# Performance work log

Measured on AMD Instinct MI355X. Metric: run time of the kernel, lower is better.

## Reference

```python
import jax, jax.numpy as jnp
import numpy as np

HIDDEN = 1024
N_EXPERTS = 8
TOP_K = 2
INTER = 1408
NORM_TOPK = False


def setup_inputs() -> dict:
    key = jax.random.key(0)
    ks = jax.random.split(key, 5)
    B, S = 4, 2048
    scale_h = 1.0 / np.sqrt(HIDDEN)
    scale_i = 1.0 / np.sqrt(INTER)
    return {
        "hidden_states": jax.random.normal(ks[0], (B, S, HIDDEN), dtype=jnp.float32),
        "gate_w": jax.random.normal(ks[1], (N_EXPERTS, HIDDEN), dtype=jnp.float32) * scale_h,  # router
        "w_gate": jax.random.normal(ks[2], (N_EXPERTS, HIDDEN, INTER), dtype=jnp.float32) * scale_h,
        "w_up": jax.random.normal(ks[3], (N_EXPERTS, HIDDEN, INTER), dtype=jnp.float32) * scale_h,
        "w_down": jax.random.normal(ks[4], (N_EXPERTS, INTER, HIDDEN), dtype=jnp.float32) * scale_i,
    }


def reference(hidden_states, gate_w, w_gate, w_up, w_down):
    B, S, H = hidden_states.shape
    x = hidden_states.reshape(-1, H)                     # [T, H]
    T = x.shape[0]

    router_logits = x @ gate_w.T                          # [T, E]
    probs = jax.nn.softmax(router_logits.astype(jnp.float32), axis=-1)
    topk_w, topk_idx = jax.lax.top_k(probs, TOP_K)        # [T, K]
    if NORM_TOPK:
        topk_w = topk_w / jnp.sum(topk_w, axis=-1, keepdims=True)
    topk_w = topk_w.astype(x.dtype)

    # Scatter top-k weights into dense [T, E] combine weights (0 for unselected).
    weights = jnp.zeros((T, N_EXPERTS), dtype=x.dtype)
    weights = weights.at[jnp.arange(T)[:, None], topk_idx].set(topk_w)

    # Dense grouped SwiGLU over all experts; combine masks out unrouted pairs.
    g = jnp.einsum('th,ehi->eti', x, w_gate)              # [E, T, I]
    u = jnp.einsum('th,ehi->eti', x, w_up)                # [E, T, I]
    y = jnp.einsum('eti,eih->eth', jax.nn.silu(g) * u, w_down)  # [E, T, H]
    final = jnp.einsum('eth,te->th', y, weights)          # [T, H]

    return final.reshape(B, S, H), router_logits
```

## Files before the change

### kernel.cpp

```cpp
#include <hip/hip_runtime.h>
#include <hip/hip_bf16.h>
#include <math.h>

#define T_TOK 8192
#define HID   1024
#define NE    8
#define TOPKN 2
#define INTER 1408
#define NROWS (T_TOK*TOPKN)
#define MAXWL 144
#define RBLK  256

typedef __attribute__((ext_vector_type(8))) __bf16 bf16x8;
typedef __attribute__((ext_vector_type(4))) float f32x4;
typedef __attribute__((ext_vector_type(4))) unsigned int u32x4;

__device__ __forceinline__ unsigned short f2bf(float f) {
    unsigned int u = __builtin_bit_cast(unsigned int, f);
    unsigned int lsb = (u >> 16) & 1u;
    u += 0x7fffu + lsb;
    return (unsigned short)(u >> 16);
}

__device__ __forceinline__ void gl2lds16(const void* g, void* l) {
    __builtin_amdgcn_global_load_lds(
        (const __attribute__((address_space(1))) unsigned int*)g,
        (__attribute__((address_space(3))) unsigned int*)l, 16, 0, 0);
}

__global__ __launch_bounds__(256) void moe_router(
    const float* __restrict__ x, const float* __restrict__ gate_w,
    unsigned short* __restrict__ xb, float* __restrict__ logits_out,
    int* __restrict__ topk_idx, float* __restrict__ topk_w,
    int* __restrict__ hist_g)
{
    __shared__ int lh[NE];
    int tid = threadIdx.x, wave = tid >> 6, lane = tid & 63;
    if (tid < NE) lh[tid] = 0;
    __syncthreads();

#pragma unroll 1
    for (int i = 0; i < 8; i++) {
        int t = blockIdx.x * 32 + wave * 8 + i;
        const float4* xr = (const float4*)(x + (size_t)t * HID);
        float acc[NE];
#pragma unroll
        for (int e = 0; e < NE; e++) acc[e] = 0.f;
#pragma unroll
        for (int j = 0; j < 4; j++) {
            float4 xv = xr[j * 64 + lane];
            ushort4 pk;
            pk.x = f2bf(xv.x); pk.y = f2bf(xv.y);
            pk.z = f2bf(xv.z); pk.w = f2bf(xv.w);
            *(ushort4*)(xb + (size_t)t * HID + j * 256 + lane * 4) = pk;
#pragma unroll
            for (int e = 0; e < NE; e++) {
                float4 gv = *(const float4*)(gate_w + e * HID + j * 256 + lane * 4);
                acc[e] += xv.x * gv.x + xv.y * gv.y + xv.z * gv.z + xv.w * gv.w;
            }
        }
#pragma unroll
        for (int e = 0; e < NE; e++) {
            float v = acc[e];
#pragma unroll
            for (int off = 32; off; off >>= 1) v += __shfl_xor(v, off, 64);
            acc[e] = v;
        }
        if (lane == 0) {
            float m = acc[0];
#pragma unroll
            for (int e = 1; e < NE; e++) m = fmaxf(m, acc[e]);
            float p[NE]; float s = 0.f;
#pragma unroll
            for (int e = 0; e < NE; e++) { p[e] = expf(acc[e] - m); s += p[e]; }
            float inv = 1.f / s;
#pragma unroll
            for (int e = 0; e < NE; e++) logits_out[(size_t)t * NE + e] = acc[e];
            int i0 = 0;
#pragma unroll
            for (int e = 1; e < NE; e++) if (p[e] > p[i0]) i0 = e;
            int i1 = (i0 == 0) ? 1 : 0;
#pragma unroll
            for (int e = 0; e < NE; e++) if (e != i0 && p[e] > p[i1]) i1 = e;
            topk_idx[2 * t]     = i0; topk_w[2 * t]     = p[i0] * inv;
            topk_idx[2 * t + 1] = i1; topk_w[2 * t + 1] = p[i1] * inv;
            atomicAdd(&lh[i0], 1);
            atomicAdd(&lh[i1], 1);
        }
    }
    __syncthreads();
    if (tid < NE) hist_g[blockIdx.x * NE + tid] = lh[tid];
}

__global__ __launch_bounds__(256) void moe_scan(
    const int* __restrict__ hist_g, int* __restrict__ offsets,
    int* __restrict__ block_base, int* __restrict__ wl, int* __restrict__ n_wl)
{
    __shared__ int h[RBLK * NE];
    __shared__ int cnt[NE], offs[NE];
    int tid = threadIdx.x;
    for (int i = tid; i < RBLK * NE; i += 256) h[i] = hist_g[i];
    __syncthreads();
    if (tid < NE) {
        int s = 0;
        for (int b = 0; b < RBLK; b++) s += h[b * NE + tid];
        cnt[tid] = s;
    }
    __syncthreads();
    if (tid == 0) {
        int s = 0;
        for (int e = 0; e < NE; e++) { offs[e] = s; offsets[e] = s; s += cnt[e]; }
        offsets[NE] = s;
        int n = 0;
        for (int e = 0; e < NE; e++)
            for (int r0 = 0; r0 < cnt[e]; r0 += 128)
                wl[n++] = (e << 24) | r0;
        *n_wl = n;
    }
    __syncthreads();
    if (tid < NE) {
        int run = offs[tid];
        for (int b = 0; b < RBLK; b++) {
            block_base[b * NE + tid] = run;
            run += h[b * NE + tid];
        }
    }
}

__global__ __launch_bounds__(64) void moe_scatter(
    const int* __restrict__ topk_idx, const float* __restrict__ topk_w,
    const int* __restrict__ block_base, int* __restrict__ row_token,
    float* __restrict__ row_w, int* __restrict__ tok_rows)
{
    __shared__ int base[NE];
    int tid = threadIdx.x;
    if (tid < NE) base[tid] = block_base[blockIdx.x * NE + tid];
    __syncthreads();
    int idx = blockIdx.x * 64 + tid;
    int e = topk_idx[idx];
    int pos = atomicAdd(&base[e], 1);
    row_token[pos] = idx >> 1;
    row_w[pos] = topk_w[idx];
    tok_rows[idx] = pos;
}

__global__ __launch_bounds__(256) void moe_transpose_cast(
    const float* __restrict__ in, unsigned short* __restrict__ out,
    int R_, int C_)
{
    __shared__ float tile[32][33];
    int e = blockIdx.z;
    const float* ine = in + (size_t)e * R_ * C_;
    unsigned short* oute = out + (size_t)e * R_ * C_;
    int c0 = blockIdx.x * 32, r0 = blockIdx.y * 32;
    int tx = threadIdx.x, ty = threadIdx.y;
#pragma unroll
    for (int j = 0; j < 4; j++) {
        int r = r0 + ty + j * 8;
        tile[ty + j * 8][tx] = ine[(size_t)r * C_ + c0 + tx];
    }
    __syncthreads();
#pragma unroll
    for (int j = 0; j < 4; j++) {
        int c = c0 + ty + j * 8;
        oute[(size_t)c * R_ + r0 + tx] = f2bf(tile[tx][ty + j * 8]);
    }
}

__global__ __launch_bounds__(256) void moe_gemm1(
    const unsigned short* __restrict__ xb,
    const unsigned short* __restrict__ wg_t,
    const unsigned short* __restrict__ wu_t,
    const int* __restrict__ offsets, const int* __restrict__ row_token,
    const int* __restrict__ wl, const int* __restrict__ n_wl,
    unsigned short* __restrict__ h_buf)
{
    if ((int)blockIdx.y >= *n_wl) return;
    int wle = wl[blockIdx.y];
    int e = wle >> 24, row0 = wle & 0xffffff;
    int off = offsets[e], cnt = offsets[e + 1] - off;
    int i0 = blockIdx.x * 64;

    __shared__ __align__(16) unsigned short As[128 * 64];
    __shared__ __align__(16) unsigned short Bg[64 * 64];
    __shared__ __align__(16) unsigned short Bu[64 * 64];

    int tid = threadIdx.x, wave = tid >> 6, lane = tid & 63;
    int wm = wave & 1, wn = wave >> 1;
    int l16 = lane & 15, quad = lane >> 4;
    int r_ = lane >> 3, c_ = lane & 7;
    int sw = l16 & 7;

    const unsigned short* asrc[4];
#pragma unroll
    for (int it = 0; it < 4; it++) {
        int rloc = it * 32 + wave * 8 + r_;
        int rg = row0 + rloc;
        int tok = row_token[off + ((rg < cnt) ? rg : 0)];
        asrc[it] = xb + (size_t)tok * HID + (c_ ^ (rloc & 7)) * 8;
    }
    const unsigned short* bgsrc[2];
    const unsigned short* busrc[2];
#pragma unroll
    for (int it = 0; it < 2; it++) {
        int rloc = it * 32 + wave * 8 + r_;
        size_t boff = (size_t)e * INTER * HID + (size_t)(i0 + rloc) * HID + (c_ ^ (rloc & 7)) * 8;
        bgsrc[it] = wg_t + boff;
        busrc[it] = wu_t + boff;
    }

    f32x4 accg[4][2], accu[4][2];
#pragma unroll
    for (int mi = 0; mi < 4; mi++)
#pragma unroll
        for (int ni = 0; ni < 2; ni++) {
            accg[mi][ni] = {0.f, 0.f, 0.f, 0.f};
            accu[mi][ni] = {0.f, 0.f, 0.f, 0.f};
        }

    for (int k0 = 0; k0 < HID; k0 += 64) {
#pragma unroll
        for (int it = 0; it < 4; it++)
            gl2lds16(asrc[it] + k0, &As[(it * 32 + wave * 8) * 64]);
#pragma unroll
        for (int it = 0; it < 2; it++) {
            gl2lds16(bgsrc[it] + k0, &Bg[(it * 32 + wave * 8) * 64]);
            gl2lds16(busrc[it] + k0, &Bu[(it * 32 + wave * 8) * 64]);
        }
        __syncthreads();
#pragma unroll
        for (int kk8 = 0; kk8 < 8; kk8 += 4) {
            int q = kk8 + quad;
            int qs = (q ^ sw) * 8;
            bf16x8 a[4], bg[2], bu[2];
#pragma unroll
            for (int mi = 0; mi < 4; mi++)
                a[mi] = *(const bf16x8*)&As[(wm * 64 + mi * 16 + l16) * 64 + qs];
#pragma unroll
            for (int ni = 0; ni < 2; ni++) {
                bg[ni] = *(const bf16x8*)&Bg[(wn * 32 + ni * 16 + l16) * 64 + qs];
                bu[ni] = *(const bf16x8*)&Bu[(wn * 32 + ni * 16 + l16) * 64 + qs];
            }
#pragma unroll
            for (int mi = 0; mi < 4; mi++)
#pragma unroll
                for (int ni = 0; ni < 2; ni++) {
                    accg[mi][ni] = __builtin_amdgcn_mfma_f32_16x16x32_bf16(a[mi], bg[ni], accg[mi][ni], 0, 0, 0);
                    accu[mi][ni] = __builtin_amdgcn_mfma_f32_16x16x32_bf16(a[mi], bu[ni], accu[mi][ni], 0, 0, 0);
                }
        }
        __syncthreads();
    }
#pragma unroll
    for (int mi = 0; mi < 4; mi++)
#pragma unroll
        for (int ni = 0; ni < 2; ni++)
#pragma unroll
            for (int r = 0; r < 4; r++) {
                int ml = wm * 64 + mi * 16 + quad * 4 + r;
                int row = row0 + ml;
                if (row < cnt) {
                    float g = accg[mi][ni][r], u = accu[mi][ni][r];
                    float hv = (g / (1.f + expf(-g))) * u;
                    h_buf[(size_t)(off + row) * INTER + i0 + wn * 32 + ni * 16 + l16] = f2bf(hv);
                }
            }
}

__global__ __launch_bounds__(256) void moe_gemm2(
    const unsigned short* __restrict__ h_buf,
    const unsigned short* __restrict__ wd_t,
    const int* __restrict__ offsets, const float* __restrict__ row_w,
    const int* __restrict__ wl, const int* __restrict__ n_wl,
    unsigned short* __restrict__ y_buf)
{
    if ((int)blockIdx.y >= *n_wl) return;
    int wle = wl[blockIdx.y];
    int e = wle >> 24, row0 = wle & 0xffffff;
    int off = offsets[e], cnt = offsets[e + 1] - off;
    int h0 = blockIdx.x * 128;

    __shared__ __align__(16) unsigned short As[128 * 64];
    __shared__ __align__(16) unsigned short Bs[128 * 64];

    int tid = threadIdx.x, wave = tid >> 6, lane = tid & 63;
    int wm = wave & 1, wn = wave >> 1;
    int l16 = lane & 15, quad = lane >> 4;
    int r_ = lane >> 3, c_ = lane & 7;
    int sw = l16 & 7;

    const unsigned short* asrc[4];
    const unsigned short* bsrc[4];
#pragma unroll
    for (int it = 0; it < 4; it++) {
        int rloc = it * 32 + wave * 8 + r_;
        int rg = row0 + rloc;
        asrc[it] = h_buf + (size_t)(off + ((rg < cnt) ? rg : 0)) * INTER + (c_ ^ (rloc & 7)) * 8;
        bsrc[it] = wd_t + (size_t)e * HID * INTER + (size_t)(h0 + rloc) * INTER + (c_ ^ (rloc & 7)) * 8;
    }

    f32x4 acc[4][4];
#pragma unroll
    for (int mi = 0; mi < 4; mi++)
#pragma unroll
        for (int ni = 0; ni < 4; ni++) acc[mi][ni] = {0.f, 0.f, 0.f, 0.f};

    for (int k0 = 0; k0 < INTER; k0 += 64) {
#pragma unroll
        for (int it = 0; it < 4; it++) {
            gl2lds16(asrc[it] + k0, &As[(it * 32 + wave * 8) * 64]);
            gl2lds16(bsrc[it] + k0, &Bs[(it * 32 + wave * 8) * 64]);
        }
        __syncthreads();
#pragma unroll
        for (int kk8 = 0; kk8 < 8; kk8 += 4) {
            int q = kk8 + quad;
            int qs = (q ^ sw) * 8;
            bf16x8 a[4], b[4];
#pragma unroll
            for (int mi = 0; mi < 4; mi++)
                a[mi] = *(const bf16x8*)&As[(wm * 64 + mi * 16 + l16) * 64 + qs];
#pragma unroll
            for (int ni = 0; ni < 4; ni++)
                b[ni] = *(const bf16x8*)&Bs[(wn * 64 + ni * 16 + l16) * 64 + qs];
#pragma unroll
            for (int mi = 0; mi < 4; mi++)
#pragma unroll
                for (int ni = 0; ni < 4; ni++)
                    acc[mi][ni] = __builtin_amdgcn_mfma_f32_16x16x32_bf16(a[mi], b[ni], acc[mi][ni], 0, 0, 0);
        }
        __syncthreads();
    }
#pragma unroll
    for (int mi = 0; mi < 4; mi++)
#pragma unroll
        for (int ni = 0; ni < 4; ni++)
#pragma unroll
            for (int r = 0; r < 4; r++) {
                int ml = wm * 64 + mi * 16 + quad * 4 + r;
                int row = row0 + ml;
                if (row < cnt) {
                    float w = row_w[off + row];
                    y_buf[(size_t)(off + row) * HID + h0 + wn * 64 + ni * 16 + l16] =
                        f2bf(acc[mi][ni][r] * w);
                }
            }
}

__global__ __launch_bounds__(256) void moe_combine(
    const unsigned short* __restrict__ y_buf, const int* __restrict__ tok_rows,
    float* __restrict__ out)
{
    int gid = blockIdx.x * 256 + threadIdx.x;
    int t = gid >> 7;
    int c = gid & 127;
    u32x4 a = *(const u32x4*)(y_buf + (size_t)tok_rows[2 * t]     * HID + c * 8);
    u32x4 b = *(const u32x4*)(y_buf + (size_t)tok_rows[2 * t + 1] * HID + c * 8);
    float res[8];
#pragma unroll
    for (int j = 0; j < 4; j++) {
        unsigned int wa = a[j], wb = b[j];
        res[2 * j]     = __builtin_bit_cast(float, wa << 16)
                       + __builtin_bit_cast(float, wb << 16);
        res[2 * j + 1] = __builtin_bit_cast(float, wa & 0xffff0000u)
                       + __builtin_bit_cast(float, wb & 0xffff0000u);
    }
    float* o = out + (size_t)t * HID + c * 8;
    *(float4*)(o)     = make_float4(res[0], res[1], res[2], res[3]);
    *(float4*)(o + 4) = make_float4(res[4], res[5], res[6], res[7]);
}

extern "C" void kernel_launch(void* const* d_in, const int* in_sizes, int n_in,
                              void* d_out, int out_size, void* d_ws, size_t ws_size,
                              hipStream_t stream)
{
    const float* x      = (const float*)d_in[0];
    const float* gate_w = (const float*)d_in[1];
    const float* w_gate = (const float*)d_in[2];
    const float* w_up   = (const float*)d_in[3];
    const float* w_down = (const float*)d_in[4];
    float* out = (float*)d_out;
    float* logits_out = out + (size_t)T_TOK * HID;

    char* ws = (char*)d_ws;
    int*   offsets    = (int*)(ws + 0);
    int*   n_wl       = (int*)(ws + 64);
    int*   wl         = (int*)(ws + 128);
    int*   hist_g     = (int*)(ws + 1024);
    int*   block_base = (int*)(ws + 1024 + 8192);
    int*   topk_idx   = (int*)(ws + 32768);
    float* topk_w     = (float*)(ws + 32768 + 65536);
    int*   row_token  = (int*)(ws + 32768 + 2 * 65536);
    float* row_w      = (float*)(ws + 32768 + 3 * 65536);
    int*   tok_rows   = (int*)(ws + 32768 + 4 * 65536);
    size_t o = 32768 + 5 * (size_t)65536 + 32768;
    unsigned short* xb   = (unsigned short*)(ws + o); o += (size_t)T_TOK * HID * 2;
    unsigned short* wg_t = (unsigned short*)(ws + o); o += (size_t)NE * INTER * HID * 2;
    unsigned short* wu_t = (unsigned short*)(ws + o); o += (size_t)NE * INTER * HID * 2;
    unsigned short* wd_t = (unsigned short*)(ws + o); o += (size_t)NE * HID * INTER * 2;
    unsigned short* h_buf = (unsigned short*)(ws + o); o += (size_t)NROWS * INTER * 2;
    unsigned short* y_buf = (unsigned short*)(ws + o); o += (size_t)NROWS * HID * 2;

    moe_router<<<RBLK, 256, 0, stream>>>(x, gate_w, xb, logits_out,
                                         topk_idx, topk_w, hist_g);
    moe_scan<<<1, 256, 0, stream>>>(hist_g, offsets, block_base, wl, n_wl);
    moe_scatter<<<RBLK, 64, 0, stream>>>(topk_idx, topk_w, block_base,
                                         row_token, row_w, tok_rows);
    dim3 tb(32, 8, 1);
    moe_transpose_cast<<<dim3(INTER / 32, HID / 32, NE), tb, 0, stream>>>(w_gate, wg_t, HID, INTER);
    moe_transpose_cast<<<dim3(INTER / 32, HID / 32, NE), tb, 0, stream>>>(w_up,   wu_t, HID, INTER);
    moe_transpose_cast<<<dim3(HID / 32, INTER / 32, NE), tb, 0, stream>>>(w_down, wd_t, INTER, HID);

    moe_gemm1<<<dim3(INTER / 64, MAXWL), 256, 0, stream>>>(
        xb, wg_t, wu_t, offsets, row_token, wl, n_wl, h_buf);
    moe_gemm2<<<dim3(HID / 128, MAXWL), 256, 0, stream>>>(
        h_buf, wd_t, offsets, row_w, wl, n_wl, y_buf);
    moe_combine<<<(T_TOK * HID / 8) / 256, 256, 0, stream>>>(y_buf, tok_rows, out);
}
```

Baseline: 470.7 us.

## Merge router with weight transposes and fold scan into scatter kernel

Combines the router kernel and the three weight transpose-cast kernels into one launch, with block index selecting the role. The scan is also folded into the scatter kernel: each block recomputes its own prefix from the histogram, and block 0 writes the offsets and a padded work list. This cuts the launch count from 9 to 5 and removes the serial single-block scan. The cost is redundant histogram reduction in every scatter block, plus the GEMMs now bounds-check padded work-list entries instead of reading a count.

Measured after the change: 480.6 us. +2.1%, slower.

```diff
diff --git a/kernel.cpp b/kernel.cpp
--- a/kernel.cpp
+++ b/kernel.cpp
@@ -10,6 +10,7 @@
 #define NROWS (T_TOK*TOPKN)
 #define MAXWL 144
 #define RBLK  256
+#define TPM   (NE * 44 * 32)
 
 typedef __attribute__((ext_vector_type(8))) __bf16 bf16x8;
 typedef __attribute__((ext_vector_type(4))) float f32x4;
@@ -28,142 +29,157 @@
         (__attribute__((address_space(3))) unsigned int*)l, 16, 0, 0);
 }
 
-__global__ __launch_bounds__(256) void moe_router(
+__global__ __launch_bounds__(256) void moe_prep(
     const float* __restrict__ x, const float* __restrict__ gate_w,
+    const float* __restrict__ w_gate, const float* __restrict__ w_up,
+    const float* __restrict__ w_down,
     unsigned short* __restrict__ xb, float* __restrict__ logits_out,
     int* __restrict__ topk_idx, float* __restrict__ topk_w,
-    int* __restrict__ hist_g)
-{
+    int* __restrict__ hist_g,
+    unsigned short* __restrict__ wg_t, unsigned short* __restrict__ wu_t,
+    unsigned short* __restrict__ wd_t)
+{
+    __shared__ float tile[32][33];
     __shared__ int lh[NE];
-    int tid = threadIdx.x, wave = tid >> 6, lane = tid & 63;
-    if (tid < NE) lh[tid] = 0;
+    int bid = blockIdx.x, tid = threadIdx.x;
+
+    if (bid < RBLK) {
+        int wave = tid >> 6, lane = tid & 63;
+        if (tid < NE) lh[tid] = 0;
+        __syncthreads();
+#pragma unroll 1
+        for (int i = 0; i < 8; i++) {
+            int t = bid * 32 + wave * 8 + i;
+            const float4* xr = (const float4*)(x + (size_t)t * HID);
+            float acc[NE];
+#pragma unroll
+            for (int e = 0; e < NE; e++) acc[e] = 0.f;
+#pragma unroll
+            for (int j = 0; j < 4; j++) {
+                float4 xv = xr[j * 64 + lane];
+                ushort4 pk;
+                pk.x = f2bf(xv.x); pk.y = f2bf(xv.y);
+                pk.z = f2bf(xv.z); pk.w = f2bf(xv.w);
+                *(ushort4*)(xb + (size_t)t * HID + j * 256 + lane * 4) = pk;
+#pragma unroll
+                for (int e = 0; e < NE; e++) {
+                    float4 gv = *(const float4*)(gate_w + e * HID + j * 256 + lane * 4);
+                    acc[e] += xv.x * gv.x + xv.y * gv.y + xv.z * gv.z + xv.w * gv.w;
+                }
+            }
+#pragma unroll
+            for (int e = 0; e < NE; e++) {
+                float v = acc[e];
+#pragma unroll
+                for (int off = 32; off; off >>= 1) v += __shfl_xor(v, off, 64);
+                acc[e] = v;
+            }
+            if (lane == 0) {
+                float m = acc[0];
+#pragma unroll
+                for (int e = 1; e < NE; e++) m = fmaxf(m, acc[e]);
+                float p[NE]; float s = 0.f;
+#pragma unroll
+                for (int e = 0; e < NE; e++) { p[e] = expf(acc[e] - m); s += p[e]; }
+                float inv = 1.f / s;
+#pragma unroll
+                for (int e = 0; e < NE; e++) logits_out[(size_t)t * NE + e] = acc[e];
+                int i0 = 0;
+#pragma unroll
+                for (int e = 1; e < NE; e++) if (p[e] > p[i0]) i0 = e;
+                int i1 = (i0 == 0) ? 1 : 0;
+#pragma unroll
+                for (int e = 0; e < NE; e++) if (e != i0 && p[e] > p[i1]) i1 = e;
+                topk_idx[2 * t]     = i0; topk_w[2 * t]     = p[i0] * inv;
+                topk_idx[2 * t + 1] = i1; topk_w[2 * t + 1] = p[i1] * inv;
+                atomicAdd(&lh[i0], 1);
+                atomicAdd(&lh[i1], 1);
+            }
+        }
+        __syncthreads();
+        if (tid < NE) hist_g[bid * NE + tid] = lh[tid];
+        return;
+    }
+
+    int t = bid - RBLK;
+    int mat = t / TPM, rem = t % TPM;
+    int e = rem / (44 * 32), r2 = rem % (44 * 32);
+    const float* in; unsigned short* outp; int R_, C_, cx, cy;
+    if (mat < 2) {
+        R_ = HID; C_ = INTER; cx = r2 % 44; cy = r2 / 44;
+        in = mat ? w_up : w_gate; outp = mat ? wu_t : wg_t;
+    } else {
+        R_ = INTER; C_ = HID; cx = r2 % 32; cy = r2 / 32;
+        in = w_down; outp = wd_t;
+    }
+    const float* ine = in + (size_t)e * R_ * C_;
+    unsigned short* oute = outp + (size_t)e * R_ * C_;
+    int c0 = cx * 32, r0 = cy * 32;
+    int tx = tid & 31, ty = tid >> 5;
+#pragma unroll
+    for (int j = 0; j < 4; j++) {
+        int r = r0 + ty + j * 8;
+        tile[ty + j * 8][tx] = ine[(size_t)r * C_ + c0 + tx];
+    }
     __syncthreads();
-
-#pragma unroll 1
-    for (int i = 0; i < 8; i++) {
-        int t = blockIdx.x * 32 + wave * 8 + i;
-        const float4* xr = (const float4*)(x + (size_t)t * HID);
-        float acc[NE];
-#pragma unroll
-        for (int e = 0; e < NE; e++) acc[e] = 0.f;
-#pragma unroll
-        for (int j = 0; j < 4; j++) {
-            float4 xv = xr[j * 64 + lane];
-            ushort4 pk;
-            pk.x = f2bf(xv.x); pk.y = f2bf(xv.y);
-            pk.z = f2bf(xv.z); pk.w = f2bf(xv.w);
-            *(ushort4*)(xb + (size_t)t * HID + j * 256 + lane * 4) = pk;
-#pragma unroll
-            for (int e = 0; e < NE; e++) {
-                float4 gv = *(const float4*)(gate_w + e * HID + j * 256 + lane * 4);
-                acc[e] += xv.x * gv.x + xv.y * gv.y + xv.z * gv.z + xv.w * gv.w;
-            }
-        }
-#pragma unroll
-        for (int e = 0; e < NE; e++) {
-            float v = acc[e];
-#pragma unroll
-            for (int off = 32; off; off >>= 1) v += __shfl_xor(v, off, 64);
-            acc[e] = v;
-        }
-        if (lane == 0) {
-            float m = acc[0];
-#pragma unroll
-            for (int e = 1; e < NE; e++) m = fmaxf(m, acc[e]);
-            float p[NE]; float s = 0.f;
-#pragma unroll
-            for (int e = 0; e < NE; e++) { p[e] = expf(acc[e] - m); s += p[e]; }
-            float inv = 1.f / s;
-#pragma unroll
-            for (int e = 0; e < NE; e++) logits_out[(size_t)t * NE + e] = acc[e];
-            int i0 = 0;
-#pragma unroll
-            for (int e = 1; e < NE; e++) if (p[e] > p[i0]) i0 = e;
-            int i1 = (i0 == 0) ? 1 : 0;
-#pragma unroll
-            for (int e = 0; e < NE; e++) if (e != i0 && p[e] > p[i1]) i1 = e;
-            topk_idx[2 * t]     = i0; topk_w[2 * t]     = p[i0] * inv;
-            topk_idx[2 * t + 1] = i1; topk_w[2 * t + 1] = p[i1] * inv;
-            atomicAdd(&lh[i0], 1);
-            atomicAdd(&lh[i1], 1);
-        }
-    }
-    __syncthreads();
-    if (tid < NE) hist_g[blockIdx.x * NE + tid] = lh[tid];
-}
-
-__global__ __launch_bounds__(256) void moe_scan(
-    const int* __restrict__ hist_g, int* __restrict__ offsets,
-    int* __restrict__ block_base, int* __restrict__ wl, int* __restrict__ n_wl)
+#pragma unroll
+    for (int j = 0; j < 4; j++) {
+        int c = c0 + ty + j * 8;
+        oute[(size_t)c * R_ + r0 + tx] = f2bf(tile[tx][ty + j * 8]);
+    }
+}
+
+__global__ __launch_bounds__(256) void moe_scatter_scan(
+    const int* __restrict__ hist_g, const int* __restrict__ topk_idx,
+    const float* __restrict__ topk_w,
+    int* __restrict__ offsets, int* __restrict__ wl,
+    int* __restrict__ row_token, float* __restrict__ row_w,
+    int* __restrict__ tok_rows)
 {
     __shared__ int h[RBLK * NE];
-    __shared__ int cnt[NE], offs[NE];
+    __shared__ int base[NE], cnt[NE];
     int tid = threadIdx.x;
     for (int i = tid; i < RBLK * NE; i += 256) h[i] = hist_g[i];
     __syncthreads();
     if (tid < NE) {
-        int s = 0;
-        for (int b = 0; b < RBLK; b++) s += h[b * NE + tid];
+        int b0 = blockIdx.x;
+        int s = 0, bb = 0;
+        for (int b = 0; b < RBLK; b++) {
+            int v = h[b * NE + tid];
+            s += v;
+            if (b < b0) bb += v;
+        }
         cnt[tid] = s;
-    }
-    __syncthreads();
-    if (tid == 0) {
-        int s = 0;
-        for (int e = 0; e < NE; e++) { offs[e] = s; offsets[e] = s; s += cnt[e]; }
-        offsets[NE] = s;
-        int n = 0;
-        for (int e = 0; e < NE; e++)
-            for (int r0 = 0; r0 < cnt[e]; r0 += 128)
-                wl[n++] = (e << 24) | r0;
-        *n_wl = n;
+        base[tid] = bb;
     }
     __syncthreads();
     if (tid < NE) {
-        int run = offs[tid];
-        for (int b = 0; b < RBLK; b++) {
-            block_base[b * NE + tid] = run;
-            run += h[b * NE + tid];
-        }
-    }
-}
-
-__global__ __launch_bounds__(64) void moe_scatter(
-    const int* __restrict__ topk_idx, const float* __restrict__ topk_w,
-    const int* __restrict__ block_base, int* __restrict__ row_token,
-    float* __restrict__ row_w, int* __restrict__ tok_rows)
-{
-    __shared__ int base[NE];
-    int tid = threadIdx.x;
-    if (tid < NE) base[tid] = block_base[blockIdx.x * NE + tid];
+        int off = 0;
+        for (int e = 0; e < tid; e++) off += cnt[e];
+        base[tid] += off;
+    }
+    if (blockIdx.x == 0) {
+        if (tid == 64) {
+            int s = 0;
+            for (int e = 0; e < NE; e++) { offsets[e] = s; s += cnt[e]; }
+            offsets[NE] = s;
+        }
+        if (tid == 128) {
+            int n = 0;
+            for (int e = 0; e < NE; e++)
+                for (int r0 = 0; r0 < cnt[e]; r0 += 128)
+                    wl[n++] = (e << 24) | r0;
+            while (n < MAXWL) wl[n++] = 0x00ffffff;
+        }
+    }
     __syncthreads();
-    int idx = blockIdx.x * 64 + tid;
-    int e = topk_idx[idx];
-    int pos = atomicAdd(&base[e], 1);
-    row_token[pos] = idx >> 1;
-    row_w[pos] = topk_w[idx];
-    tok_rows[idx] = pos;
-}
-
-__global__ __launch_bounds__(256) void moe_transpose_cast(
-    const float* __restrict__ in, unsigned short* __restrict__ out,
-    int R_, int C_)
-{
-    __shared__ float tile[32][33];
-    int e = blockIdx.z;
-    const float* ine = in + (size_t)e * R_ * C_;
-    unsigned short* oute = out + (size_t)e * R_ * C_;
-    int c0 = blockIdx.x * 32, r0 = blockIdx.y * 32;
-    int tx = threadIdx.x, ty = threadIdx.y;
-#pragma unroll
-    for (int j = 0; j < 4; j++) {
-        int r = r0 + ty + j * 8;
-        tile[ty + j * 8][tx] = ine[(size_t)r * C_ + c0 + tx];
-    }
-    __syncthreads();
-#pragma unroll
-    for (int j = 0; j < 4; j++) {
-        int c = c0 + ty + j * 8;
-        oute[(size_t)c * R_ + r0 + tx] = f2bf(tile[tx][ty + j * 8]);
+    if (tid < 64) {
+        int idx = blockIdx.x * 64 + tid;
+        int e = topk_idx[idx];
+        int pos = atomicAdd(&base[e], 1);
+        row_token[pos] = idx >> 1;
+        row_w[pos] = topk_w[idx];
+        tok_rows[idx] = pos;
     }
 }
 
@@ -172,13 +188,13 @@
     const unsigned short* __restrict__ wg_t,
     const unsigned short* __restrict__ wu_t,
     const int* __restrict__ offsets, const int* __restrict__ row_token,
-    const int* __restrict__ wl, const int* __restrict__ n_wl,
+    const int* __restrict__ wl,
     unsigned short* __restrict__ h_buf)
 {
-    if ((int)blockIdx.y >= *n_wl) return;
     int wle = wl[blockIdx.y];
     int e = wle >> 24, row0 = wle & 0xffffff;
     int off = offsets[e], cnt = offsets[e + 1] - off;
+    if (row0 >= cnt) return;
     int i0 = blockIdx.x * 64;
 
     __shared__ __align__(16) unsigned short As[128 * 64];
@@ -271,13 +287,13 @@
     const unsigned short* __restrict__ h_buf,
     const unsigned short* __restrict__ wd_t,
     const int* __restrict__ offsets, const float* __restrict__ row_w,
-    const int* __restrict__ wl, const int* __restrict__ n_wl,
+    const int* __restrict__ wl,
     unsigned short* __restrict__ y_buf)
 {
-    if ((int)blockIdx.y >= *n_wl) return;
     int wle = wl[blockIdx.y];
     int e = wle >> 24, row0 = wle & 0xffffff;
     int off = offsets[e], cnt = offsets[e + 1] - off;
+    if (row0 >= cnt) return;
     int h0 = blockIdx.x * 128;
 
     __shared__ __align__(16) unsigned short As[128 * 64];
@@ -384,10 +400,8 @@
 
     char* ws = (char*)d_ws;
     int*   offsets    = (int*)(ws + 0);
-    int*   n_wl       = (int*)(ws + 64);
     int*   wl         = (int*)(ws + 128);
     int*   hist_g     = (int*)(ws + 1024);
-    int*   block_base = (int*)(ws + 1024 + 8192);
     int*   topk_idx   = (int*)(ws + 32768);
     float* topk_w     = (float*)(ws + 32768 + 65536);
     int*   row_token  = (int*)(ws + 32768 + 2 * 65536);
@@ -401,19 +415,14 @@
     unsigned short* h_buf = (unsigned short*)(ws + o); o += (size_t)NROWS * INTER * 2;
     unsigned short* y_buf = (unsigned short*)(ws + o); o += (size_t)NROWS * HID * 2;
 
-    moe_router<<<RBLK, 256, 0, stream>>>(x, gate_w, xb, logits_out,
-                                         topk_idx, topk_w, hist_g);
-    moe_scan<<<1, 256, 0, stream>>>(hist_g, offsets, block_base, wl, n_wl);
-    moe_scatter<<<RBLK, 64, 0, stream>>>(topk_idx, topk_w, block_base,
-                                         row_token, row_w, tok_rows);
-    dim3 tb(32, 8, 1);
-    moe_transpose_cast<<<dim3(INTER / 32, HID / 32, NE), tb, 0, stream>>>(w_gate, wg_t, HID, INTER);
-    moe_transpose_cast<<<dim3(INTER / 32, HID / 32, NE), tb, 0, stream>>>(w_up,   wu_t, HID, INTER);
-    moe_transpose_cast<<<dim3(HID / 32, INTER / 32, NE), tb, 0, stream>>>(w_down, wd_t, INTER, HID);
-
+    moe_prep<<<RBLK + 3 * TPM, 256, 0, stream>>>(
+        x, gate_w, w_gate, w_up, w_down,
+        xb, logits_out, topk_idx, topk_w, hist_g, wg_t, wu_t, wd_t);
+    moe_scatter_scan<<<RBLK, 256, 0, stream>>>(
+        hist_g, topk_idx, topk_w, offsets, wl, row_token, row_w, tok_rows);
     moe_gemm1<<<dim3(INTER / 64, MAXWL), 256, 0, stream>>>(
-        xb, wg_t, wu_t, offsets, row_token, wl, n_wl, h_buf);
+        xb, wg_t, wu_t, offsets, row_token, wl, h_buf);
     moe_gemm2<<<dim3(HID / 128, MAXWL), 256, 0, stream>>>(
-        h_buf, wd_t, offsets, row_w, wl, n_wl, y_buf);
+        h_buf, wd_t, offsets, row_w, wl, y_buf);
     moe_combine<<<(T_TOK * HID / 8) / 256, 256, 0, stream>>>(y_buf, tok_rows, out);
 }
```
